# Performance work log

Hardware: AMD Instinct MI355X
Metric: run time of the kernel (lower is better)

Reference implementation:

```python
import jax, jax.numpy as jnp
import numpy as np

N_EMBED = 1024
N_HEADS = 16
HEAD_SIZE = N_EMBED // N_HEADS
BLOCK_SIZE = 256
LN_EPS = 1e-5


def _layernorm(x, g, b):
    mu = jnp.mean(x, axis=-1, keepdims=True)
    var = jnp.var(x, axis=-1, keepdims=True)
    return (x - mu) * jax.lax.rsqrt(var + LN_EPS) * g + b


def setup_inputs() -> dict:
    key = jax.random.key(0)
    ks = jax.random.split(key, 12)
    B, T, C, H, D = 64, 256, N_EMBED, N_HEADS, HEAD_SIZE
    s = lambda fan_in: 1.0 / np.sqrt(fan_in)
    return {
        "x": jax.random.normal(ks[0], (B, T, C), jnp.float32),
        # per-head Q/K/V projections (bias=False in torch), stacked over heads
        "Wq": jax.random.uniform(ks[1], (H, C, D), jnp.float32, -s(C), s(C)),
        "Wk": jax.random.uniform(ks[2], (H, C, D), jnp.float32, -s(C), s(C)),
        "Wv": jax.random.uniform(ks[3], (H, C, D), jnp.float32, -s(C), s(C)),
        "Wproj": jax.random.uniform(ks[4], (C, C), jnp.float32, -s(C), s(C)),
        "bproj": jax.random.uniform(ks[5], (C,), jnp.float32, -s(C), s(C)),
        "W1": jax.random.uniform(ks[6], (C, 4 * C), jnp.float32, -s(C), s(C)),
        "b1": jax.random.uniform(ks[7], (4 * C,), jnp.float32, -s(C), s(C)),
        "W2": jax.random.uniform(ks[8], (4 * C, C), jnp.float32, -s(4 * C), s(4 * C)),
        "b2": jax.random.uniform(ks[9], (C,), jnp.float32, -s(4 * C), s(4 * C)),
        "ln1_g": jnp.ones((C,), jnp.float32),
        "ln1_b": jnp.zeros((C,), jnp.float32),
        "ln2_g": jnp.ones((C,), jnp.float32),
        "ln2_b": jnp.zeros((C,), jnp.float32),
    }


def reference(x, Wq, Wk, Wv, Wproj, bproj, W1, b1, W2, b2, ln1_g, ln1_b, ln2_g, ln2_b):
    B, T, C = x.shape
    # --- self-attention sub-block ---
    h = _layernorm(x, ln1_g, ln1_b)
    q = jnp.einsum("btc,hcd->bhtd", h, Wq)
    k = jnp.einsum("btc,hcd->bhtd", h, Wk)
    v = jnp.einsum("btc,hcd->bhtd", h, Wv)
    # NOTE: original scales by C**-0.5 with C = n_embed (full dim), not head_size
    scores = jnp.einsum("bhtd,bhsd->bhts", q, k) * (C ** -0.5)
    causal = jnp.tril(jnp.ones((T, T), bool))
    scores = jnp.where(causal, scores, -jnp.inf)
    wei = jax.nn.softmax(scores, axis=-1)
    attn = jnp.einsum("bhts,bhsd->bhtd", wei, v)  # [B,H,T,D]
    attn = attn.transpose(0, 2, 1, 3).reshape(B, T, C)  # concat heads
    x = x + attn @ Wproj + bproj
    # --- feed-forward sub-block ---
    h2 = _layernorm(x, ln2_g, ln2_b)
    ffn = jax.nn.relu(h2 @ W1 + b1) @ W2 + b2
    return x + ffn
```

## Files before the change

kernel.cpp:

```cpp
#include <hip/hip_runtime.h>
#include <stdint.h>

using u16 = unsigned short;
using u32 = unsigned int;

typedef __attribute__((ext_vector_type(8))) short s16x8;
typedef __attribute__((ext_vector_type(4))) float f32x4;

__device__ __forceinline__ float bf2f(u16 u) { u32 t = (u32)u << 16; float f; __builtin_memcpy(&f, &t, 4); return f; }
__device__ __forceinline__ u16 f2bf(float f) {
  u32 u; __builtin_memcpy(&u, &f, 4);
  return (u16)((u + 0x7fffu + ((u >> 16) & 1u)) >> 16);
}

__device__ __forceinline__ void gload_lds16(const void* g, void* l) {
  __builtin_amdgcn_global_load_lds((const __attribute__((address_space(1))) void*)g,
                                   (__attribute__((address_space(3))) void*)l, 16, 0, 0);
}

__global__ __launch_bounds__(256)
void transpose_pack(const float* __restrict__ in, u16* __restrict__ out,
                    int R, int Cc, long in_bs, long out_bs)
{
  __shared__ float tile[32][33];
  in  += (size_t)blockIdx.z * in_bs;
  out += (size_t)blockIdx.z * out_bs;
  const int r0 = blockIdx.x * 32, c0 = blockIdx.y * 32;
  const int tx = threadIdx.x & 31, ty = threadIdx.x >> 5;
#pragma unroll
  for (int i = 0; i < 4; ++i) {
    int r = ty + i * 8;
    tile[r][tx] = in[(size_t)(r0 + r) * Cc + c0 + tx];
  }
  __syncthreads();
#pragma unroll
  for (int i = 0; i < 4; ++i) {
    int c = ty + i * 8;
    out[(size_t)(c0 + c) * R + r0 + tx] = f2bf(tile[tx][c]);
  }
}

template <int IN>
__global__ __launch_bounds__(256)
void ln_to_bf16(const void* __restrict__ xv, const float* __restrict__ g,
                const float* __restrict__ bta, u16* __restrict__ out)
{
  const int row = blockIdx.x, tid = threadIdx.x;
  float4 v;
  if constexpr (IN == 0) {
    v = ((const float4*)((const float*)xv + (size_t)row * 1024))[tid];
  } else {
    uint2 u = ((const uint2*)((const u16*)xv + (size_t)row * 1024))[tid];
    v.x = bf2f((u16)(u.x & 0xffff)); v.y = bf2f((u16)(u.x >> 16));
    v.z = bf2f((u16)(u.y & 0xffff)); v.w = bf2f((u16)(u.y >> 16));
  }
  float s  = v.x + v.y + v.z + v.w;
  float ss = v.x * v.x + v.y * v.y + v.z * v.z + v.w * v.w;
#pragma unroll
  for (int m = 1; m < 64; m <<= 1) {
    s  += __shfl_xor(s, m);
    ss += __shfl_xor(ss, m);
  }
  __shared__ float red[8];
  const int wave = tid >> 6, lane = tid & 63;
  if (lane == 0) { red[wave] = s; red[4 + wave] = ss; }
  __syncthreads();
  s  = red[0] + red[1] + red[2] + red[3];
  ss = red[4] + red[5] + red[6] + red[7];
  const float mu  = s * (1.f / 1024.f);
  const float var = ss * (1.f / 1024.f) - mu * mu;
  const float rs  = rsqrtf(var + 1e-5f);
  const float4 gg = ((const float4*)g)[tid];
  const float4 bb = ((const float4*)bta)[tid];
  u32 w0 = (u32)f2bf((v.x - mu) * rs * gg.x + bb.x) | ((u32)f2bf((v.y - mu) * rs * gg.y + bb.y) << 16);
  u32 w1 = (u32)f2bf((v.z - mu) * rs * gg.z + bb.z) | ((u32)f2bf((v.w - mu) * rs * gg.w + bb.w) << 16);
  u32* outp = (u32*)(out + (size_t)row * 1024 + tid * 4);
  outp[0] = w0; outp[1] = w1;
}

#define DSR(d, a, o) asm volatile("ds_read_b128 %0, %1 offset:" o : "=v"(d) : "v"(a))
#define ISSUE12(aR, bR) \
  DSR(bv0, bR, "0"); DSR(bv1, bR, "2048"); DSR(bv2, bR, "4096"); DSR(bv3, bR, "6144"); \
  DSR(av0, aR, "0"); DSR(av1, aR, "2048"); DSR(av2, aR, "4096"); DSR(av3, aR, "6144"); \
  DSR(av4, aR, "8192"); DSR(av5, aR, "10240"); DSR(av6, aR, "12288"); DSR(av7, aR, "14336")
#define ISSUE8(aR, bR) \
  DSR(bv0, bR, "0"); DSR(bv1, bR, "2048"); DSR(bv2, bR, "4096"); DSR(bv3, bR, "6144"); \
  DSR(av0, aR, "0"); DSR(av1, aR, "2048"); DSR(av2, aR, "4096"); DSR(av3, aR, "6144")
#define MM(m, n) acc[m][n] = __builtin_amdgcn_mfma_f32_16x16x32_bf16(av##m, bv##n, acc[m][n], 0, 0, 0)
#define RUNG(m, cnt) \
  asm volatile("s_waitcnt lgkmcnt(" #cnt ")" ::: "memory"); \
  __builtin_amdgcn_sched_barrier(0); \
  MM(m, 0); MM(m, 1); MM(m, 2); MM(m, 3)
#define LADDER12() \
  RUNG(0, 7); RUNG(1, 6); RUNG(2, 5); RUNG(3, 4); \
  RUNG(4, 3); RUNG(5, 2); RUNG(6, 1); RUNG(7, 0)

template <int EPI>
__device__ __forceinline__ void gemm_epilogue(f32x4 (&acc)[8][4], void* Cv, const float* bias,
                                              const void* resid, int N, int bm, int bn,
                                              int wr, int wc, int r, int kg)
{
#pragma unroll
  for (int m = 0; m < 8; ++m) {
#pragma unroll
    for (int n = 0; n < 4; ++n) {
#pragma unroll
      for (int j = 0; j < 4; ++j) {
        int row = bm * 256 + wr * 128 + m * 16 + kg * 4 + j;
        int col = bn * 256 + wc * 64 + n * 16 + r;
        size_t idx = (size_t)row * N + col;
        float v = acc[m][n][j];
        if constexpr (EPI == 0) {
          ((u16*)Cv)[idx] = f2bf(v);
        } else if constexpr (EPI == 1) {
          ((u16*)Cv)[idx] = f2bf(v + bias[col] + ((const float*)resid)[idx]);
        } else if constexpr (EPI == 2) {
          ((u16*)Cv)[idx] = f2bf(fmaxf(v + bias[col], 0.f));
        } else {
          ((float*)Cv)[idx] = v + bias[col] + bf2f(((const u16*)resid)[idx]);
        }
      }
    }
  }
}

template <int EPI>
__global__ __launch_bounds__(512, 2)
void gemm8p(const u16* __restrict__ A, const u16* __restrict__ B, void* __restrict__ Cv,
            const float* __restrict__ bias, const void* __restrict__ resid,
            int M, int N, int K, int CM, int CN, int XN)
{
  __shared__ u16 lds[65536];
  const int NT = K >> 6;
  const int tid = threadIdx.x;
  const int lane = tid & 63, wv = tid >> 6;
  const int wr = wv >> 2, wc = wv & 3;
  const int r = lane & 15, kg = lane >> 4;

  const int bid = blockIdx.x;
  const int x = bid & 7, i = bid >> 3;
  const int bm = (x / XN) * CM + i / CN;
  const int bn = (x % XN) * CN + i % CN;

  const u16* Ab = A + (size_t)bm * 256 * K;
  const u16* Bb = B + (size_t)bn * 256 * K;

  const u32 ldsb = (u32)(uintptr_t)lds;
  const u32 segb = (u32)((kg ^ (r >> 1)) << 4);
  const u32 abase = ldsb + (u32)((wr * 128 + r) * 128) + segb;
  const u32 bbase = ldsb + 65536u + (u32)((wc * 64 + r) * 128) + segb;

  f32x4 acc[8][4];
#pragma unroll
  for (int m = 0; m < 8; ++m)
#pragma unroll
    for (int n = 0; n < 4; ++n) acc[m][n] = f32x4{0.f, 0.f, 0.f, 0.f};

  auto stage = [&](const u16* src, int u, int h, int base_u16) {
#pragma unroll
    for (int jj = 0; jj < 2; ++jj) {
      int ci = jj * 512 + tid;
      int rl = ci >> 3;
      int sseg = (ci & 7) ^ ((rl >> 1) & 7);
      gload_lds16(src + (size_t)(h * 128 + rl) * K + u * 64 + sseg * 8,
                  &lds[base_u16 + h * 8192 + ci * 8]);
    }
  };

  stage(Ab, 0, 0, 0);      stage(Ab, 0, 1, 0);
  stage(Bb, 0, 0, 32768);  stage(Bb, 0, 1, 32768);
  asm volatile("s_waitcnt vmcnt(0)" ::: "memory");
  __builtin_amdgcn_s_barrier();

  for (int t = 0; t < NT; ++t) {
    const int buf = t & 1;
    const bool s1 = (t + 1) < NT;
    const int nb = (buf ^ 1) * 16384;
    const u32 aA0 = abase + (u32)(buf * 32768);
    const u32 aB0 = bbase + (u32)(buf * 32768);

    if (s1) {
      stage(Ab, t + 1, 0, nb);           stage(Ab, t + 1, 1, nb);
      stage(Bb, t + 1, 0, 32768 + nb);   stage(Bb, t + 1, 1, 32768 + nb);
    }
    __builtin_amdgcn_sched_barrier(0);
    __builtin_amdgcn_s_setprio(1);
    {
      s16x8 av0, av1, av2, av3, av4, av5, av6, av7, bv0, bv1, bv2, bv3;
      ISSUE12(aA0, aB0);
      LADDER12();
    }
    {
      s16x8 av0, av1, av2, av3, av4, av5, av6, av7, bv0, bv1, bv2, bv3;
      ISSUE12(aA0 ^ 64u, aB0 ^ 64u);
      LADDER12();
    }
    __builtin_amdgcn_s_setprio(0);
    __builtin_amdgcn_sched_barrier(0);
    asm volatile("s_waitcnt vmcnt(0)" ::: "memory");
    __builtin_amdgcn_s_barrier();
  }
  gemm_epilogue<EPI>(acc, Cv, bias, resid, N, bm, bn, wr, wc, r, kg);
}

template <int EPI>
__global__ __launch_bounds__(256, 4)
void gemm1s(const u16* __restrict__ A, const u16* __restrict__ B, void* __restrict__ Cv,
            const float* __restrict__ bias, const void* __restrict__ resid,
            int M, int N, int K, int CM, int CN, int XN)
{
  __shared__ u16 lds[16384];
  const int NT = K >> 6;
  const int tid = threadIdx.x;
  const int lane = tid & 63, wv = tid >> 6;
  const int wr = wv >> 1, wc = wv & 1;
  const int r = lane & 15, kg = lane >> 4;

  const int bid = blockIdx.x;
  const int x = bid & 7, i = bid >> 3;
  const int bm = (x / XN) * CM + i / CN;
  const int bn = (x % XN) * CN + i % CN;

  const u16* Ab = A + (size_t)bm * 128 * K;
  const u16* Bb = B + (size_t)bn * 128 * K;

  const u32 ldsb = (u32)(uintptr_t)lds;
  const u32 segb = (u32)((kg ^ (r >> 1)) << 4);
  const u32 aA0 = ldsb + (u32)((wr * 64 + r) * 128) + segb;
  const u32 aB0 = ldsb + 16384u + (u32)((wc * 64 + r) * 128) + segb;

  f32x4 acc[4][4];
#pragma unroll
  for (int m = 0; m < 4; ++m)
#pragma unroll
    for (int n = 0; n < 4; ++n) acc[m][n] = f32x4{0.f, 0.f, 0.f, 0.f};

  auto stage = [&](const u16* src, int u, int base_u16) {
#pragma unroll
    for (int jj = 0; jj < 4; ++jj) {
      int ci = jj * 256 + tid;
      int rl = ci >> 3;
      int sseg = (ci & 7) ^ ((rl >> 1) & 7);
      gload_lds16(src + (size_t)rl * K + u * 64 + sseg * 8, &lds[base_u16 + ci * 8]);
    }
  };

  stage(Ab, 0, 0);
  stage(Bb, 0, 8192);
  asm volatile("s_waitcnt vmcnt(0)" ::: "memory");
  __builtin_amdgcn_s_barrier();

  for (int t = 0; t < NT; ++t) {
    const bool s1 = (t + 1) < NT;
    __builtin_amdgcn_s_setprio(1);
    {
      s16x8 av0, av1, av2, av3, bv0, bv1, bv2, bv3;
      ISSUE8(aA0, aB0);
      RUNG(0, 3); RUNG(1, 2); RUNG(2, 1); RUNG(3, 0);
    }
    {
      s16x8 av0, av1, av2, av3, bv0, bv1, bv2, bv3;
      ISSUE8(aA0 ^ 64u, aB0 ^ 64u);
      RUNG(0, 3); RUNG(1, 2); RUNG(2, 1);
      asm volatile("s_waitcnt lgkmcnt(0)" ::: "memory");
      __builtin_amdgcn_sched_barrier(0);
      __builtin_amdgcn_s_setprio(0);
      __builtin_amdgcn_s_barrier();
      __builtin_amdgcn_sched_barrier(0);
      if (s1) {
        stage(Ab, t + 1, 0);
        stage(Bb, t + 1, 8192);
      }
      __builtin_amdgcn_sched_barrier(0);
      __builtin_amdgcn_s_setprio(1);
      MM(3, 0); MM(3, 1); MM(3, 2); MM(3, 3);
    }
    __builtin_amdgcn_s_setprio(0);
    __builtin_amdgcn_sched_barrier(0);
    asm volatile("s_waitcnt vmcnt(0)" ::: "memory");
    __builtin_amdgcn_s_barrier();
  }

#pragma unroll
  for (int m = 0; m < 4; ++m) {
#pragma unroll
    for (int n = 0; n < 4; ++n) {
#pragma unroll
      for (int j = 0; j < 4; ++j) {
        int row = bm * 128 + wr * 64 + m * 16 + kg * 4 + j;
        int col = bn * 128 + wc * 64 + n * 16 + r;
        size_t idx = (size_t)row * N + col;
        float v = acc[m][n][j];
        if constexpr (EPI == 0) {
          ((u16*)Cv)[idx] = f2bf(v);
        } else if constexpr (EPI == 1) {
          ((u16*)Cv)[idx] = f2bf(v + bias[col] + ((const float*)resid)[idx]);
        } else if constexpr (EPI == 2) {
          ((u16*)Cv)[idx] = f2bf(fmaxf(v + bias[col], 0.f));
        } else {
          ((float*)Cv)[idx] = v + bias[col] + bf2f(((const u16*)resid)[idx]);
        }
      }
    }
  }
}

#undef DSR
#undef ISSUE12
#undef ISSUE8
#undef MM
#undef RUNG
#undef LADDER12

__global__ __launch_bounds__(256)
void attn_mfma(const u16* __restrict__ qkv, u16* __restrict__ outc)
{
  const int bh = blockIdx.x, b = bh >> 4, h = bh & 15;
  const int tid = threadIdx.x;
  const int lane = tid & 63, w = tid >> 6;
  const int r = lane & 15, kg = lane >> 4;

  __shared__ u16 Ks[64 * 64];
  __shared__ u16 Vt[64 * 72];
  __shared__ u16 P[4][64 * 72];

  const u16* qbase = qkv + (size_t)(b * 256) * 3072 + h * 64;

  s16x8 qf[4][2];
#pragma unroll
  for (int m = 0; m < 4; ++m)
#pragma unroll
    for (int ks = 0; ks < 2; ++ks)
      qf[m][ks] = *(const s16x8*)(qbase + (size_t)(w * 64 + m * 16 + r) * 3072 + ks * 32 + kg * 8);

  f32x4 of[4][4];
  float mrun[4][4], lrun[4][4];
#pragma unroll
  for (int m = 0; m < 4; ++m) {
#pragma unroll
    for (int n = 0; n < 4; ++n) of[m][n] = f32x4{0.f, 0.f, 0.f, 0.f};
#pragma unroll
    for (int j = 0; j < 4; ++j) { mrun[m][j] = -1e30f; lrun[m][j] = 0.f; }
  }

  const float cexp = 0.03125f * 1.4426950408889634f;

  for (int kt = 0; kt < 4; ++kt) {
#pragma unroll
    for (int jj = 0; jj < 2; ++jj) {
      int ci = jj * 256 + tid;
      int key = ci >> 3, seg = ci & 7;
      int sseg = seg ^ (key & 7);
      gload_lds16(qkv + (size_t)(b * 256 + kt * 64 + key) * 3072 + 1024 + h * 64 + sseg * 8,
                  &Ks[ci * 8]);
    }
    {
      int row = tid >> 2, q = tid & 3;
      const u16* vg = qkv + (size_t)(b * 256 + kt * 64 + row) * 3072 + 2048 + h * 64 + q * 16;
      union { uint4 u[2]; u16 s[16]; } vv;
      vv.u[0] = *(const uint4*)vg;
      vv.u[1] = *(const uint4*)(vg + 8);
#pragma unroll
      for (int i = 0; i < 16; ++i)
        Vt[(q * 16 + i) * 72 + row] = vv.s[i];
    }
    __syncthreads();

    if (w >= kt) {
      f32x4 s[4][4];
#pragma unroll
      for (int m = 0; m < 4; ++m)
#pragma unroll
        for (int n = 0; n < 4; ++n) s[m][n] = f32x4{0.f, 0.f, 0.f, 0.f};
#pragma unroll
      for (int ks = 0; ks < 2; ++ks) {
        s16x8 kb[4];
#pragma unroll
        for (int n = 0; n < 4; ++n) {
          int row = n * 16 + r;
          int sseg = (ks * 4 + kg) ^ (row & 7);
          kb[n] = *(const s16x8*)&Ks[row * 64 + sseg * 8];
        }
#pragma unroll
        for (int m = 0; m < 4; ++m)
#pragma unroll
          for (int n = 0; n < 4; ++n)
            s[m][n] = __builtin_amdgcn_mfma_f32_16x16x32_bf16(qf[m][ks], kb[n], s[m][n], 0, 0, 0);
      }
      if (kt == w) {
#pragma unroll
        for (int m = 0; m < 4; ++m)
#pragma unroll
          for (int n = 0; n < 4; ++n)
#pragma unroll
            for (int j = 0; j < 4; ++j)
              if (n * 16 + r > m * 16 + kg * 4 + j) s[m][n][j] = -1e30f;
      }
#pragma unroll
      for (int m = 0; m < 4; ++m) {
        float rm[4], rsc[4], ls[4];
#pragma unroll
        for (int j = 0; j < 4; ++j) {
          rm[j] = fmaxf(fmaxf(s[m][0][j], s[m][1][j]), fmaxf(s[m][2][j], s[m][3][j]));
          rm[j] = fmaxf(rm[j], __shfl_xor(rm[j], 1));
          rm[j] = fmaxf(rm[j], __shfl_xor(rm[j], 2));
          rm[j] = fmaxf(rm[j], __shfl_xor(rm[j], 4));
          rm[j] = fmaxf(rm[j], __shfl_xor(rm[j], 8));
          float mnew = fmaxf(mrun[m][j], rm[j]);
          rsc[j] = exp2f((mrun[m][j] - mnew) * cexp);
          mrun[m][j] = mnew;
          ls[j] = 0.f;
        }
#pragma unroll
        for (int n = 0; n < 4; ++n)
#pragma unroll
          for (int j = 0; j < 4; ++j) {
            float p = exp2f((s[m][n][j] - mrun[m][j]) * cexp);
            ls[j] += p;
            P[w][(m * 16 + kg * 4 + j) * 72 + n * 16 + r] = f2bf(p);
          }
#pragma unroll
        for (int j = 0; j < 4; ++j) {
          ls[j] += __shfl_xor(ls[j], 1);
          ls[j] += __shfl_xor(ls[j], 2);
          ls[j] += __shfl_xor(ls[j], 4);
          ls[j] += __shfl_xor(ls[j], 8);
          lrun[m][j] = lrun[m][j] * rsc[j] + ls[j];
        }
#pragma unroll
        for (int n = 0; n < 4; ++n)
#pragma unroll
          for (int j = 0; j < 4; ++j)
            of[m][n][j] *= rsc[j];
      }
#pragma unroll
      for (int kk = 0; kk < 2; ++kk) {
        s16x8 pa[4], vb[4];
#pragma unroll
        for (int m = 0; m < 4; ++m)
          pa[m] = *(const s16x8*)&P[w][(m * 16 + r) * 72 + kk * 32 + kg * 8];
#pragma unroll
        for (int n = 0; n < 4; ++n)
          vb[n] = *(const s16x8*)&Vt[(n * 16 + r) * 72 + kk * 32 + kg * 8];
#pragma unroll
        for (int m = 0; m < 4; ++m)
#pragma unroll
          for (int n = 0; n < 4; ++n)
            of[m][n] = __builtin_amdgcn_mfma_f32_16x16x32_bf16(pa[m], vb[n], of[m][n], 0, 0, 0);
      }
    }
    __syncthreads();
  }

#pragma unroll
  for (int m = 0; m < 4; ++m) {
    float inv[4];
#pragma unroll
    for (int j = 0; j < 4; ++j) inv[j] = 1.f / lrun[m][j];
#pragma unroll
    for (int n = 0; n < 4; ++n)
#pragma unroll
      for (int j = 0; j < 4; ++j) {
        int row = b * 256 + w * 64 + m * 16 + kg * 4 + j;
        outc[(size_t)row * 1024 + h * 64 + n * 16 + r] = f2bf(of[m][n][j] * inv[j]);
      }
  }
}

extern "C" void kernel_launch(void* const* d_in, const int* in_sizes, int n_in,
                              void* d_out, int out_size, void* d_ws, size_t ws_size,
                              hipStream_t stream) {
  (void)in_sizes; (void)n_in; (void)out_size; (void)ws_size;
  const float* x     = (const float*)d_in[0];
  const float* Wq    = (const float*)d_in[1];
  const float* Wk    = (const float*)d_in[2];
  const float* Wv    = (const float*)d_in[3];
  const float* Wproj = (const float*)d_in[4];
  const float* bproj = (const float*)d_in[5];
  const float* W1    = (const float*)d_in[6];
  const float* b1    = (const float*)d_in[7];
  const float* W2    = (const float*)d_in[8];
  const float* b2    = (const float*)d_in[9];
  const float* ln1g  = (const float*)d_in[10];
  const float* ln1b  = (const float*)d_in[11];
  const float* ln2g  = (const float*)d_in[12];
  const float* ln2b  = (const float*)d_in[13];
  float* out = (float*)d_out;

  char* ws = (char*)d_ws;
  u16*   WqkvT  = (u16*)(ws + 0);
  u16*   WprojT = (u16*)(ws + 6291456);
  u16*   W1T    = (u16*)(ws + 8388608);
  u16*   W2T    = (u16*)(ws + 16777216);
  u16*   hb     = (u16*)(ws + 25165824);
  u16*   qkvb   = (u16*)(ws + 58720256);
  u16*   x2     = (u16*)(ws + 159383552);
  u16*   h2     = (u16*)(ws + 226492416);
  u16*   ffn1   = (u16*)(ws + 25165824);
  u16*   attnout = hb;

  const int M = 16384;

  transpose_pack<<<dim3(32, 2, 16), 256, 0, stream>>>(Wq, WqkvT,           1024, 64, 65536, 65536);
  transpose_pack<<<dim3(32, 2, 16), 256, 0, stream>>>(Wk, WqkvT + 1048576, 1024, 64, 65536, 65536);
  transpose_pack<<<dim3(32, 2, 16), 256, 0, stream>>>(Wv, WqkvT + 2097152, 1024, 64, 65536, 65536);
  transpose_pack<<<dim3(32, 32, 1), 256, 0, stream>>>(Wproj, WprojT, 1024, 1024, 0, 0);
  transpose_pack<<<dim3(32, 128, 1), 256, 0, stream>>>(W1, W1T, 1024, 4096, 0, 0);
  transpose_pack<<<dim3(128, 32, 1), 256, 0, stream>>>(W2, W2T, 4096, 1024, 0, 0);

  ln_to_bf16<0><<<M, 256, 0, stream>>>(x, ln1g, ln1b, hb);

  gemm8p<0><<<768, 512, 0, stream>>>(hb, WqkvT, qkvb, nullptr, nullptr, M, 3072, 1024, 16, 6, 2);

  attn_mfma<<<1024, 256, 0, stream>>>(qkvb, attnout);

  gemm8p<1><<<256, 512, 0, stream>>>(attnout, WprojT, x2, bproj, x, M, 1024, 1024, 8, 4, 1);

  ln_to_bf16<1><<<M, 256, 0, stream>>>(x2, ln2g, ln2b, h2);

  gemm1s<2><<<4096, 256, 0, stream>>>(h2, W1T, ffn1, b1, nullptr, M, 4096, 1024, 64, 8, 4);

  gemm1s<3><<<1024, 256, 0, stream>>>(ffn1, W2T, out, b2, x2, M, 1024, 4096, 16, 8, 1);
}
```

Before: 568.2 us.

## Split attention into one-wave blocks per query tile and use gemm8p for FFN1

The attention kernel is restructured from one 4-wave block per (batch, head) into 4096 single-wave blocks, one per 64-row query tile. Each block loops only over the causal key tiles, which removes block-wide syncs and the idle waves in early tiles, and relies on more blocks to balance load. The trade-off is that each wave loads K/V on its own, so the same K/V tiles are read from global memory several times. The FFN1 GEMM is also switched from gemm1s to the gemm8p kernel with a 512-thread configuration.

New measurement: 597.2 us. 5.1% more time.

```diff
diff --git a/kernel.cpp b/kernel.cpp
--- a/kernel.cpp
+++ b/kernel.cpp
@@ -312,17 +312,19 @@
 #undef RUNG
 #undef LADDER12
 
-__global__ __launch_bounds__(256)
-void attn_mfma(const u16* __restrict__ qkv, u16* __restrict__ outc)
+__global__ __launch_bounds__(64)
+void attn_1w(const u16* __restrict__ qkv, u16* __restrict__ outc)
 {
-  const int bh = blockIdx.x, b = bh >> 4, h = bh & 15;
-  const int tid = threadIdx.x;
-  const int lane = tid & 63, w = tid >> 6;
+  const int bid = blockIdx.x;
+  const int qt = bid & 3;
+  const int h  = (bid >> 2) & 15;
+  const int b  = bid >> 6;
+  const int lane = threadIdx.x;
   const int r = lane & 15, kg = lane >> 4;
 
   __shared__ u16 Ks[64 * 64];
   __shared__ u16 Vt[64 * 72];
-  __shared__ u16 P[4][64 * 72];
+  __shared__ u16 P[64 * 72];
 
   const u16* qbase = qkv + (size_t)(b * 256) * 3072 + h * 64;
 
@@ -331,7 +333,7 @@
   for (int m = 0; m < 4; ++m)
 #pragma unroll
     for (int ks = 0; ks < 2; ++ks)
-      qf[m][ks] = *(const s16x8*)(qbase + (size_t)(w * 64 + m * 16 + r) * 3072 + ks * 32 + kg * 8);
+      qf[m][ks] = *(const s16x8*)(qbase + (size_t)(qt * 64 + m * 16 + r) * 3072 + ks * 32 + kg * 8);
 
   f32x4 of[4][4];
   float mrun[4][4], lrun[4][4];
@@ -345,111 +347,108 @@
 
   const float cexp = 0.03125f * 1.4426950408889634f;
 
-  for (int kt = 0; kt < 4; ++kt) {
-#pragma unroll
-    for (int jj = 0; jj < 2; ++jj) {
-      int ci = jj * 256 + tid;
+  for (int kt = 0; kt <= qt; ++kt) {
+#pragma unroll
+    for (int jj = 0; jj < 8; ++jj) {
+      int ci = jj * 64 + lane;
       int key = ci >> 3, seg = ci & 7;
       int sseg = seg ^ (key & 7);
       gload_lds16(qkv + (size_t)(b * 256 + kt * 64 + key) * 3072 + 1024 + h * 64 + sseg * 8,
                   &Ks[ci * 8]);
     }
     {
-      int row = tid >> 2, q = tid & 3;
-      const u16* vg = qkv + (size_t)(b * 256 + kt * 64 + row) * 3072 + 2048 + h * 64 + q * 16;
-      union { uint4 u[2]; u16 s[16]; } vv;
-      vv.u[0] = *(const uint4*)vg;
-      vv.u[1] = *(const uint4*)(vg + 8);
-#pragma unroll
-      for (int i = 0; i < 16; ++i)
-        Vt[(q * 16 + i) * 72 + row] = vv.s[i];
-    }
-    __syncthreads();
-
-    if (w >= kt) {
-      f32x4 s[4][4];
+      const uint4* vg = (const uint4*)(qkv + (size_t)(b * 256 + kt * 64 + lane) * 3072 + 2048 + h * 64);
+      union { uint4 u[8]; u16 s[64]; } vv;
+#pragma unroll
+      for (int j = 0; j < 8; ++j) vv.u[j] = vg[j];
+#pragma unroll
+      for (int i = 0; i < 64; ++i)
+        Vt[i * 72 + lane] = vv.s[i];
+    }
+    asm volatile("s_waitcnt vmcnt(0) lgkmcnt(0)" ::: "memory");
+    __builtin_amdgcn_sched_barrier(0);
+
+    f32x4 s[4][4];
+#pragma unroll
+    for (int m = 0; m < 4; ++m)
+#pragma unroll
+      for (int n = 0; n < 4; ++n) s[m][n] = f32x4{0.f, 0.f, 0.f, 0.f};
+#pragma unroll
+    for (int ks = 0; ks < 2; ++ks) {
+      s16x8 kb[4];
+#pragma unroll
+      for (int n = 0; n < 4; ++n) {
+        int row = n * 16 + r;
+        int sseg = (ks * 4 + kg) ^ (row & 7);
+        kb[n] = *(const s16x8*)&Ks[row * 64 + sseg * 8];
+      }
 #pragma unroll
       for (int m = 0; m < 4; ++m)
 #pragma unroll
-        for (int n = 0; n < 4; ++n) s[m][n] = f32x4{0.f, 0.f, 0.f, 0.f};
-#pragma unroll
-      for (int ks = 0; ks < 2; ++ks) {
-        s16x8 kb[4];
-#pragma unroll
-        for (int n = 0; n < 4; ++n) {
-          int row = n * 16 + r;
-          int sseg = (ks * 4 + kg) ^ (row & 7);
-          kb[n] = *(const s16x8*)&Ks[row * 64 + sseg * 8];
+        for (int n = 0; n < 4; ++n)
+          s[m][n] = __builtin_amdgcn_mfma_f32_16x16x32_bf16(qf[m][ks], kb[n], s[m][n], 0, 0, 0);
+    }
+    if (kt == qt) {
+#pragma unroll
+      for (int m = 0; m < 4; ++m)
+#pragma unroll
+        for (int n = 0; n < 4; ++n)
+#pragma unroll
+          for (int j = 0; j < 4; ++j)
+            if (n * 16 + r > m * 16 + kg * 4 + j) s[m][n][j] = -1e30f;
+    }
+#pragma unroll
+    for (int m = 0; m < 4; ++m) {
+      float rm[4], rsc[4], ls[4];
+#pragma unroll
+      for (int j = 0; j < 4; ++j) {
+        rm[j] = fmaxf(fmaxf(s[m][0][j], s[m][1][j]), fmaxf(s[m][2][j], s[m][3][j]));
+        rm[j] = fmaxf(rm[j], __shfl_xor(rm[j], 1));
+        rm[j] = fmaxf(rm[j], __shfl_xor(rm[j], 2));
+        rm[j] = fmaxf(rm[j], __shfl_xor(rm[j], 4));
+        rm[j] = fmaxf(rm[j], __shfl_xor(rm[j], 8));
+        float mnew = fmaxf(mrun[m][j], rm[j]);
+        rsc[j] = exp2f((mrun[m][j] - mnew) * cexp);
+        mrun[m][j] = mnew;
+        ls[j] = 0.f;
+      }
+#pragma unroll
+      for (int n = 0; n < 4; ++n)
+#pragma unroll
+        for (int j = 0; j < 4; ++j) {
+          float p = exp2f((s[m][n][j] - mrun[m][j]) * cexp);
+          ls[j] += p;
+          P[(m * 16 + kg * 4 + j) * 72 + n * 16 + r] = f2bf(p);
         }
 #pragma unroll
-        for (int m = 0; m < 4; ++m)
-#pragma unroll
-          for (int n = 0; n < 4; ++n)
-            s[m][n] = __builtin_amdgcn_mfma_f32_16x16x32_bf16(qf[m][ks], kb[n], s[m][n], 0, 0, 0);
-      }
-      if (kt == w) {
-#pragma unroll
-        for (int m = 0; m < 4; ++m)
-#pragma unroll
-          for (int n = 0; n < 4; ++n)
-#pragma unroll
-            for (int j = 0; j < 4; ++j)
-              if (n * 16 + r > m * 16 + kg * 4 + j) s[m][n][j] = -1e30f;
-      }
-#pragma unroll
-      for (int m = 0; m < 4; ++m) {
-        float rm[4], rsc[4], ls[4];
-#pragma unroll
-        for (int j = 0; j < 4; ++j) {
-          rm[j] = fmaxf(fmaxf(s[m][0][j], s[m][1][j]), fmaxf(s[m][2][j], s[m][3][j]));
-          rm[j] = fmaxf(rm[j], __shfl_xor(rm[j], 1));
-          rm[j] = fmaxf(rm[j], __shfl_xor(rm[j], 2));
-          rm[j] = fmaxf(rm[j], __shfl_xor(rm[j], 4));
-          rm[j] = fmaxf(rm[j], __shfl_xor(rm[j], 8));
-          float mnew = fmaxf(mrun[m][j], rm[j]);
-          rsc[j] = exp2f((mrun[m][j] - mnew) * cexp);
-          mrun[m][j] = mnew;
-          ls[j] = 0.f;
-        }
+      for (int j = 0; j < 4; ++j) {
+        ls[j] += __shfl_xor(ls[j], 1);
+        ls[j] += __shfl_xor(ls[j], 2);
+        ls[j] += __shfl_xor(ls[j], 4);
+        ls[j] += __shfl_xor(ls[j], 8);
+        lrun[m][j] = lrun[m][j] * rsc[j] + ls[j];
+      }
+#pragma unroll
+      for (int n = 0; n < 4; ++n)
+#pragma unroll
+        for (int j = 0; j < 4; ++j)
+          of[m][n][j] *= rsc[j];
+    }
+#pragma unroll
+    for (int kk = 0; kk < 2; ++kk) {
+      s16x8 pa[4], vb[4];
+#pragma unroll
+      for (int m = 0; m < 4; ++m)
+        pa[m] = *(const s16x8*)&P[(m * 16 + r) * 72 + kk * 32 + kg * 8];
+#pragma unroll
+      for (int n = 0; n < 4; ++n)
+        vb[n] = *(const s16x8*)&Vt[(n * 16 + r) * 72 + kk * 32 + kg * 8];
+#pragma unroll
+      for (int m = 0; m < 4; ++m)
 #pragma unroll
         for (int n = 0; n < 4; ++n)
-#pragma unroll
-          for (int j = 0; j < 4; ++j) {
-            float p = exp2f((s[m][n][j] - mrun[m][j]) * cexp);
-            ls[j] += p;
-            P[w][(m * 16 + kg * 4 + j) * 72 + n * 16 + r] = f2bf(p);
-          }
-#pragma unroll
-        for (int j = 0; j < 4; ++j) {
-          ls[j] += __shfl_xor(ls[j], 1);
-          ls[j] += __shfl_xor(ls[j], 2);
-          ls[j] += __shfl_xor(ls[j], 4);
-          ls[j] += __shfl_xor(ls[j], 8);
-          lrun[m][j] = lrun[m][j] * rsc[j] + ls[j];
-        }
-#pragma unroll
-        for (int n = 0; n < 4; ++n)
-#pragma unroll
-          for (int j = 0; j < 4; ++j)
-            of[m][n][j] *= rsc[j];
-      }
-#pragma unroll
-      for (int kk = 0; kk < 2; ++kk) {
-        s16x8 pa[4], vb[4];
-#pragma unroll
-        for (int m = 0; m < 4; ++m)
-          pa[m] = *(const s16x8*)&P[w][(m * 16 + r) * 72 + kk * 32 + kg * 8];
-#pragma unroll
-        for (int n = 0; n < 4; ++n)
-          vb[n] = *(const s16x8*)&Vt[(n * 16 + r) * 72 + kk * 32 + kg * 8];
-#pragma unroll
-        for (int m = 0; m < 4; ++m)
-#pragma unroll
-          for (int n = 0; n < 4; ++n)
-            of[m][n] = __builtin_amdgcn_mfma_f32_16x16x32_bf16(pa[m], vb[n], of[m][n], 0, 0, 0);
-      }
-    }
-    __syncthreads();
+          of[m][n] = __builtin_amdgcn_mfma_f32_16x16x32_bf16(pa[m], vb[n], of[m][n], 0, 0, 0);
+    }
   }
 
 #pragma unroll
@@ -461,7 +460,7 @@
     for (int n = 0; n < 4; ++n)
 #pragma unroll
       for (int j = 0; j < 4; ++j) {
-        int row = b * 256 + w * 64 + m * 16 + kg * 4 + j;
+        int row = b * 256 + qt * 64 + m * 16 + kg * 4 + j;
         outc[(size_t)row * 1024 + h * 64 + n * 16 + r] = f2bf(of[m][n][j] * inv[j]);
       }
   }
@@ -512,13 +511,13 @@
 
   gemm8p<0><<<768, 512, 0, stream>>>(hb, WqkvT, qkvb, nullptr, nullptr, M, 3072, 1024, 16, 6, 2);
 
-  attn_mfma<<<1024, 256, 0, stream>>>(qkvb, attnout);
+  attn_1w<<<4096, 64, 0, stream>>>(qkvb, attnout);
 
   gemm8p<1><<<256, 512, 0, stream>>>(attnout, WprojT, x2, bproj, x, M, 1024, 1024, 8, 4, 1);
 
   ln_to_bf16<1><<<M, 256, 0, stream>>>(x2, ln2g, ln2b, h2);
 
-  gemm1s<2><<<4096, 256, 0, stream>>>(h2, W1T, ffn1, b1, nullptr, M, 4096, 1024, 64, 8, 4);
+  gemm8p<2><<<1024, 512, 0, stream>>>(h2, W1T, ffn1, b1, nullptr, M, 4096, 1024, 16, 8, 2);
 
   gemm1s<3><<<1024, 256, 0, stream>>>(ffn1, W2T, out, b2, x2, M, 1024, 4096, 16, 8, 1);
 }
```

## Merge weight transposes and LN1 into one prologue; use gemm8p for FFN1

Applied to the files above, without the earlier changes.

Folds the six weight transpose/pack launches and the first layernorm into a single prologue kernel that picks its task from the block index, removing six launches and their serialization gaps. Separately, the first FFN GEMM moves from the gemm1s kernel to the gemm8p kernel (512 threads, different tiling parameters). That only works if gemm8p handles the bias+ReLU epilogue for mode 2, and the larger grid-task kernel mixes two very different block workloads.

Result: no change. 562.0 us, median of 2 (-1.1%).

```diff
diff --git a/kernel.cpp b/kernel.cpp
--- a/kernel.cpp
+++ b/kernel.cpp
@@ -19,14 +19,71 @@
 }
 
 __global__ __launch_bounds__(256)
-void transpose_pack(const float* __restrict__ in, u16* __restrict__ out,
-                    int R, int Cc, long in_bs, long out_bs)
+void prologue(const float* __restrict__ Wq, const float* __restrict__ Wk,
+              const float* __restrict__ Wv, const float* __restrict__ Wproj,
+              const float* __restrict__ W1, const float* __restrict__ W2,
+              u16* __restrict__ WqkvT, u16* __restrict__ WprojT,
+              u16* __restrict__ W1T, u16* __restrict__ W2T,
+              const float* __restrict__ x, const float* __restrict__ g,
+              const float* __restrict__ bta, u16* __restrict__ hb)
 {
   __shared__ float tile[32][33];
-  in  += (size_t)blockIdx.z * in_bs;
-  out += (size_t)blockIdx.z * out_bs;
-  const int r0 = blockIdx.x * 32, c0 = blockIdx.y * 32;
-  const int tx = threadIdx.x & 31, ty = threadIdx.x >> 5;
+  __shared__ float red[8];
+  int bid = blockIdx.x;
+  const int tid = threadIdx.x;
+
+  if (bid < 16384) {
+    const float4 v = ((const float4*)(x + (size_t)bid * 1024))[tid];
+    float s  = v.x + v.y + v.z + v.w;
+    float ss = v.x * v.x + v.y * v.y + v.z * v.z + v.w * v.w;
+#pragma unroll
+    for (int m = 1; m < 64; m <<= 1) {
+      s  += __shfl_xor(s, m);
+      ss += __shfl_xor(ss, m);
+    }
+    const int wave = tid >> 6, lane = tid & 63;
+    if (lane == 0) { red[wave] = s; red[4 + wave] = ss; }
+    __syncthreads();
+    s  = red[0] + red[1] + red[2] + red[3];
+    ss = red[4] + red[5] + red[6] + red[7];
+    const float mu  = s * (1.f / 1024.f);
+    const float var = ss * (1.f / 1024.f) - mu * mu;
+    const float rs  = rsqrtf(var + 1e-5f);
+    const float4 gg = ((const float4*)g)[tid];
+    const float4 bb = ((const float4*)bta)[tid];
+    u32 w0 = (u32)f2bf((v.x - mu) * rs * gg.x + bb.x) | ((u32)f2bf((v.y - mu) * rs * gg.y + bb.y) << 16);
+    u32 w1 = (u32)f2bf((v.z - mu) * rs * gg.z + bb.z) | ((u32)f2bf((v.w - mu) * rs * gg.w + bb.w) << 16);
+    u32* outp = (u32*)(hb + (size_t)bid * 1024 + tid * 4);
+    outp[0] = w0; outp[1] = w1;
+    return;
+  }
+  bid -= 16384;
+
+  const float* in; u16* out; int R, Cc, bx, by;
+  if (bid < 3072) {
+    int which = bid >> 10, r2 = bid & 1023;
+    bx = r2 & 31;
+    int rest = r2 >> 5;
+    by = rest & 1;
+    int z = rest >> 1;
+    in  = (which == 0 ? Wq : which == 1 ? Wk : Wv) + (size_t)z * 65536;
+    out = WqkvT + (size_t)which * 1048576 + (size_t)z * 65536;
+    R = 1024; Cc = 64;
+  } else if (bid < 4096) {
+    int b2 = bid - 3072;
+    bx = b2 & 31; by = b2 >> 5;
+    in = Wproj; out = WprojT; R = 1024; Cc = 1024;
+  } else if (bid < 8192) {
+    int b2 = bid - 4096;
+    bx = b2 & 31; by = b2 >> 5;
+    in = W1; out = W1T; R = 1024; Cc = 4096;
+  } else {
+    int b2 = bid - 8192;
+    bx = b2 & 127; by = b2 >> 7;
+    in = W2; out = W2T; R = 4096; Cc = 1024;
+  }
+  const int r0 = bx * 32, c0 = by * 32;
+  const int tx = tid & 31, ty = tid >> 5;
 #pragma unroll
   for (int i = 0; i < 4; ++i) {
     int r = ty + i * 8;
@@ -40,20 +97,15 @@
   }
 }
 
-template <int IN>
 __global__ __launch_bounds__(256)
-void ln_to_bf16(const void* __restrict__ xv, const float* __restrict__ g,
-                const float* __restrict__ bta, u16* __restrict__ out)
+void ln_bf16(const u16* __restrict__ xv, const float* __restrict__ g,
+             const float* __restrict__ bta, u16* __restrict__ out)
 {
   const int row = blockIdx.x, tid = threadIdx.x;
   float4 v;
-  if constexpr (IN == 0) {
-    v = ((const float4*)((const float*)xv + (size_t)row * 1024))[tid];
-  } else {
-    uint2 u = ((const uint2*)((const u16*)xv + (size_t)row * 1024))[tid];
-    v.x = bf2f((u16)(u.x & 0xffff)); v.y = bf2f((u16)(u.x >> 16));
-    v.z = bf2f((u16)(u.y & 0xffff)); v.w = bf2f((u16)(u.y >> 16));
-  }
+  uint2 u = ((const uint2*)(xv + (size_t)row * 1024))[tid];
+  v.x = bf2f((u16)(u.x & 0xffff)); v.y = bf2f((u16)(u.x >> 16));
+  v.z = bf2f((u16)(u.y & 0xffff)); v.w = bf2f((u16)(u.y >> 16));
   float s  = v.x + v.y + v.z + v.w;
   float ss = v.x * v.x + v.y * v.y + v.z * v.z + v.w * v.w;
 #pragma unroll
@@ -501,14 +553,9 @@
 
   const int M = 16384;
 
-  transpose_pack<<<dim3(32, 2, 16), 256, 0, stream>>>(Wq, WqkvT,           1024, 64, 65536, 65536);
-  transpose_pack<<<dim3(32, 2, 16), 256, 0, stream>>>(Wk, WqkvT + 1048576, 1024, 64, 65536, 65536);
-  transpose_pack<<<dim3(32, 2, 16), 256, 0, stream>>>(Wv, WqkvT + 2097152, 1024, 64, 65536, 65536);
-  transpose_pack<<<dim3(32, 32, 1), 256, 0, stream>>>(Wproj, WprojT, 1024, 1024, 0, 0);
-  transpose_pack<<<dim3(32, 128, 1), 256, 0, stream>>>(W1, W1T, 1024, 4096, 0, 0);
-  transpose_pack<<<dim3(128, 32, 1), 256, 0, stream>>>(W2, W2T, 4096, 1024, 0, 0);
-
-  ln_to_bf16<0><<<M, 256, 0, stream>>>(x, ln1g, ln1b, hb);
+  prologue<<<28672, 256, 0, stream>>>(Wq, Wk, Wv, Wproj, W1, W2,
+                                      WqkvT, WprojT, W1T, W2T,
+                                      x, ln1g, ln1b, hb);
 
   gemm8p<0><<<768, 512, 0, stream>>>(hb, WqkvT, qkvb, nullptr, nullptr, M, 3072, 1024, 16, 6, 2);
 
@@ -516,9 +563,9 @@
 
   gemm8p<1><<<256, 512, 0, stream>>>(attnout, WprojT, x2, bproj, x, M, 1024, 1024, 8, 4, 1);
 
-  ln_to_bf16<1><<<M, 256, 0, stream>>>(x2, ln2g, ln2b, h2);
-
-  gemm1s<2><<<4096, 256, 0, stream>>>(h2, W1T, ffn1, b1, nullptr, M, 4096, 1024, 64, 8, 4);
+  ln_bf16<<<M, 256, 0, stream>>>(x2, ln2g, ln2b, h2);
+
+  gemm8p<2><<<1024, 512, 0, stream>>>(h2, W1T, ffn1, b1, nullptr, M, 4096, 1024, 16, 8, 2);
 
   gemm1s<3><<<1024, 256, 0, stream>>>(ffn1, W2T, out, b2, x2, M, 1024, 4096, 16, 8, 1);
 }
```
